# Optimization experiments

Measured on AMD Instinct MI355X. Metric: run time of the kernel, lower is better.

The kernel has to match this reference:

```python
import jax, jax.numpy as jnp
import numpy as np

NUM_NODES = 100000
NODE_FEAT_DIM = 512
EDGE_FEAT_DIM = 512
MEM_DIM = NODE_FEAT_DIM + EDGE_FEAT_DIM  # 1024
BATCH = 65536


def setup_inputs() -> dict:
    key = jax.random.key(0)
    k_ids, k_mem, k_emb, kq, ks, kk = jax.random.split(key, 6)
    scale = 1.0 / np.sqrt(MEM_DIM)
    inp = {
        "node_ids": jax.random.randint(k_ids, (BATCH,), 0, NUM_NODES, dtype=jnp.int64)
        if jax.config.jax_enable_x64 else
        jax.random.randint(k_ids, (BATCH,), 0, NUM_NODES, dtype=jnp.int32),
        # memory bank: (N, 1, D); randomized (instead of the zero init) so math is non-trivial
        "node_memories": jax.random.normal(k_mem, (NUM_NODES, 1, MEM_DIM), dtype=jnp.float32) * 0.02,
        "node_embedding": jax.random.normal(k_emb, (NUM_NODES, MEM_DIM), dtype=jnp.float32) * 0.02,
        "Wq": jax.random.normal(jax.random.fold_in(kq, 0), (MEM_DIM, NODE_FEAT_DIM), dtype=jnp.float32) * scale,
        "bq": jnp.zeros((NODE_FEAT_DIM,), dtype=jnp.float32),
        "Ws": jax.random.normal(jax.random.fold_in(ks, 0), (MEM_DIM, NODE_FEAT_DIM), dtype=jnp.float32) * scale,
        "bs": jnp.zeros((NODE_FEAT_DIM,), dtype=jnp.float32),
        "Wk": jax.random.normal(jax.random.fold_in(kk, 0), (MEM_DIM, NODE_FEAT_DIM), dtype=jnp.float32) * scale,
        "bk": jnp.zeros((NODE_FEAT_DIM,), dtype=jnp.float32),
    }
    return inp


def reference(node_ids, node_memories, node_embedding, Wq, bq, Ws, bs, Wk, bk):
    ids = node_ids.astype(jnp.int32)
    # torch.sum(node_memories[ids], dim=2): reduces feature dim -> (B, 1)
    mem_sum = jnp.sum(node_memories[ids], axis=2)          # (B, 1)
    x = mem_sum + node_embedding[ids]                      # broadcast -> (B, D)
    q = jax.nn.sigmoid(x @ Wq + bq)                        # (B, node_feat_dim)
    s = jax.nn.sigmoid(x @ Ws + bs)
    k = jax.nn.sigmoid(x @ Wk + bk)
    return (q, s, k)
```

## Files before the change

kernel.cpp:

```cpp
#include <hip/hip_runtime.h>
#include <hip/hip_bf16.h>
#include <stdint.h>

#define BATCH_N 65536
#define KDIM 1024
#define NTOT 1536

typedef __bf16 bf16x8 __attribute__((ext_vector_type(8)));
typedef float f32x4 __attribute__((ext_vector_type(4)));

__device__ __forceinline__ unsigned short f2bf(float f) {
    unsigned u = __builtin_bit_cast(unsigned, f);
    u += 0x7FFFu + ((u >> 16) & 1u);
    return (unsigned short)(u >> 16);
}

__global__ __launch_bounds__(256) void prep_kernel(
    const int* __restrict__ ids,
    const float* __restrict__ mem,
    const float* __restrict__ emb,
    unsigned short* __restrict__ x)
{
    const int b    = blockIdx.x * 4 + (threadIdx.x >> 6);
    const int lane = threadIdx.x & 63;
    const int id   = ids[b];
    const float4* m4 = (const float4*)(mem + (size_t)id * KDIM) + lane;
    const float4* e4 = (const float4*)(emb + (size_t)id * KDIM) + lane;
    float4 v0 = m4[0];
    float4 v1 = m4[64];
    float4 v2 = m4[128];
    float4 v3 = m4[192];
    float s = (v0.x + v0.y + v0.z + v0.w) + (v1.x + v1.y + v1.z + v1.w)
            + (v2.x + v2.y + v2.z + v2.w) + (v3.x + v3.y + v3.z + v3.w);
    #pragma unroll
    for (int off = 1; off < 64; off <<= 1) s += __shfl_xor(s, off, 64);
    unsigned short* xb = x + (size_t)b * KDIM;
    #pragma unroll
    for (int q = 0; q < 4; ++q) {
        float4 e = e4[q * 64];
        ushort4 o;
        o.x = f2bf(s + e.x);
        o.y = f2bf(s + e.y);
        o.z = f2bf(s + e.z);
        o.w = f2bf(s + e.w);
        const int k   = q * 256 + lane * 4;
        const int ksw = k ^ ((b & 7) << 3);
        *(ushort4*)(xb + ksw) = o;
    }
}

__global__ __launch_bounds__(256) void wconv_kernel(
    const float* __restrict__ Wq, const float* __restrict__ Ws,
    const float* __restrict__ Wk, unsigned short* __restrict__ wt)
{
    const int gt = blockIdx.x * 256 + threadIdx.x;
    const int n  = gt % NTOT;
    const int kb = (gt / NTOT) * 4;
    const float* W = (n < 512) ? Wq : ((n < 1024) ? Ws : Wk);
    const int nn = n & 511;
    ushort4 o;
    o.x = f2bf(W[(size_t)(kb + 0) * 512 + nn]);
    o.y = f2bf(W[(size_t)(kb + 1) * 512 + nn]);
    o.z = f2bf(W[(size_t)(kb + 2) * 512 + nn]);
    o.w = f2bf(W[(size_t)(kb + 3) * 512 + nn]);
    const int ksw = kb ^ ((n & 7) << 3);
    *(ushort4*)(wt + (size_t)n * KDIM + ksw) = o;
}

#define BM 256
#define BN 256
#define BK 64
#define MT (BATCH_N / BM)
#define NT (NTOT / BN)
#define NWG (MT * NT)

#define BAR() asm volatile("s_barrier" ::: "memory")
#define VM0() asm volatile("s_waitcnt vmcnt(0)" ::: "memory")
#define AS1 __attribute__((address_space(1)))
#define AS3 __attribute__((address_space(3)))

__global__ __launch_bounds__(512, 2) void gemm_kernel(
    const unsigned short* __restrict__ X,
    const unsigned short* __restrict__ Wt,
    const float* __restrict__ bq, const float* __restrict__ bs,
    const float* __restrict__ bk, float* __restrict__ out)
{
    __shared__ __align__(16) unsigned short sA[32768];
    __shared__ __align__(16) unsigned short sB[32768];

    const int tid  = threadIdx.x;
    const int xcd  = blockIdx.x & 7;
    const int idx  = blockIdx.x >> 3;
    const int wgid = xcd * (NWG / 8) + idx;
    const int nt   = wgid % NT;
    const int mt   = wgid / NT;
    const int m0   = mt * BM;
    const int n0   = nt * BN;
    const int wid  = tid >> 6;
    const int lane = tid & 63;
    const int wm   = wid >> 2;
    const int wn   = wid & 3;
    const int r16  = lane & 15;
    const int kb0  = (lane >> 4) << 4;
    const int ksw  = (r16 & 7) << 4;

    f32x4 acc[8][4];
    #pragma unroll
    for (int i = 0; i < 8; i++)
        #pragma unroll
        for (int j = 0; j < 4; j++)
            acc[i][j] = f32x4{0.f, 0.f, 0.f, 0.f};

    bf16x8 af0[4][2], af1[4][2], bfr0[2][2], bfr1[2][2];

    const unsigned short* gA = X  + (size_t)(m0 + (tid >> 3)) * KDIM + (tid & 7) * 8;
    const unsigned short* gB = Wt + (size_t)(n0 + (tid >> 3)) * KDIM + (tid & 7) * 8;
    const int ldst = (tid & 448) * 8;

#define STG_A(slot, h, kt) do {                                                 \
    _Pragma("unroll")                                                            \
    for (int c = 0; c < 2; ++c)                                                  \
        __builtin_amdgcn_global_load_lds(                                        \
            (const AS1 void*)(gA + (size_t)((h) * 128 + c * 64) * KDIM + (kt) * BK), \
            (AS3 void*)(&sA[((slot) * 2 + (h)) * 8192 + c * 4096 + ldst]),       \
            16, 0, 0);                                                           \
} while (0)
#define STG_B(slot, h, kt) do {                                                 \
    _Pragma("unroll")                                                            \
    for (int c = 0; c < 2; ++c)                                                  \
        __builtin_amdgcn_global_load_lds(                                        \
            (const AS1 void*)(gB + (size_t)((h) * 128 + c * 64) * KDIM + (kt) * BK), \
            (AS3 void*)(&sB[((slot) * 2 + (h)) * 8192 + c * 4096 + ldst]),       \
            16, 0, 0);                                                           \
} while (0)

#define LDA(SET, slot, qa) do {                                                 \
    const char* p = (const char*)&sA[((slot) * 2 + (qa)) * 8192];                \
    _Pragma("unroll")                                                            \
    for (int i = 0; i < 4; ++i)                                                  \
        _Pragma("unroll")                                                        \
        for (int kk = 0; kk < 2; ++kk)                                           \
            SET[i][kk] = *(const bf16x8*)(p + (wm * 64 + i * 16 + r16) * 128     \
                                            + ((kk * 64 + kb0) ^ ksw));          \
} while (0)
#define LDB(SET, slot, qb) do {                                                 \
    const char* p = (const char*)&sB[((slot) * 2 + (qb)) * 8192];                \
    _Pragma("unroll")                                                            \
    for (int j = 0; j < 2; ++j)                                                  \
        _Pragma("unroll")                                                        \
        for (int kk = 0; kk < 2; ++kk)                                           \
            SET[j][kk] = *(const bf16x8*)(p + (wn * 32 + j * 16 + r16) * 128     \
                                            + ((kk * 64 + kb0) ^ ksw));          \
} while (0)

#define MM(QA, QB, ASET, BSET) do {                                             \
    __builtin_amdgcn_s_setprio(1);                                               \
    _Pragma("unroll")                                                            \
    for (int i = 0; i < 4; ++i)                                                  \
        _Pragma("unroll")                                                        \
        for (int j = 0; j < 2; ++j)                                              \
            _Pragma("unroll")                                                    \
            for (int kk = 0; kk < 2; ++kk)                                       \
                acc[(QA) * 4 + i][(QB) * 2 + j] =                                \
                    __builtin_amdgcn_mfma_f32_16x16x32_bf16(                     \
                        ASET[i][kk], BSET[j][kk],                                \
                        acc[(QA) * 4 + i][(QB) * 2 + j], 0, 0, 0);               \
    __builtin_amdgcn_s_setprio(0);                                               \
} while (0)

#define TILE(S, NS, KTN, DOSTAGE) do {                                          \
    if (DOSTAGE) {                                                               \
        STG_A(NS, 0, KTN); STG_A(NS, 1, KTN);                                    \
        STG_B(NS, 0, KTN); STG_B(NS, 1, KTN);                                    \
    }                                                                            \
    LDA(af0, S, 0); LDB(bfr0, S, 0);                                             \
    LDA(af1, S, 1); LDB(bfr1, S, 1);                                             \
    MM(0, 0, af0, bfr0); MM(0, 1, af0, bfr1);                                    \
    MM(1, 1, af1, bfr1); MM(1, 0, af1, bfr0);                                    \
    VM0(); BAR();                                                                \
} while (0)

    STG_A(0, 0, 0); STG_A(0, 1, 0); STG_B(0, 0, 0); STG_B(0, 1, 0);
    VM0();
    BAR();

    #pragma unroll 1
    for (int t = 0; t < 7; ++t) {
        TILE(0, 1, 2 * t + 1, 1);
        TILE(1, 0, 2 * t + 2, 1);
    }
    TILE(0, 1, 15, 1);
    TILE(1, 0, 0, 0);

    const int grp = nt >> 1;
    const float* bias = (grp == 0) ? bq : ((grp == 1) ? bs : bk);
    float* obase = out + (size_t)grp * ((size_t)BATCH_N * 512);
    const int cb = (nt & 1) * 256;
    #pragma unroll
    for (int qb = 0; qb < 2; ++qb)
        #pragma unroll
        for (int j = 0; j < 2; ++j) {
            const int col = cb + qb * 128 + wn * 32 + j * 16 + r16;
            const float bv = bias[col];
            #pragma unroll
            for (int qa = 0; qa < 2; ++qa)
                #pragma unroll
                for (int i = 0; i < 4; ++i) {
                    const int rbase = m0 + qa * 128 + wm * 64 + i * 16 + ((lane >> 4) << 2);
                    #pragma unroll
                    for (int r = 0; r < 4; ++r) {
                        float v = acc[qa * 4 + i][qb * 2 + j][r] + bv;
                        v = 1.0f / (1.0f + __expf(-v));
                        __builtin_nontemporal_store(v, &obase[(size_t)(rbase + r) * 512 + col]);
                    }
                }
        }
#undef STG_A
#undef STG_B
#undef LDA
#undef LDB
#undef MM
#undef TILE
}

extern "C" void kernel_launch(void* const* d_in, const int* in_sizes, int n_in,
                              void* d_out, int out_size, void* d_ws, size_t ws_size,
                              hipStream_t stream) {
    const int*   ids = (const int*)d_in[0];
    const float* mem = (const float*)d_in[1];
    const float* emb = (const float*)d_in[2];
    const float* Wq  = (const float*)d_in[3];
    const float* bq  = (const float*)d_in[4];
    const float* Ws  = (const float*)d_in[5];
    const float* bs  = (const float*)d_in[6];
    const float* Wk  = (const float*)d_in[7];
    const float* bk  = (const float*)d_in[8];
    float* out = (float*)d_out;

    unsigned short* x  = (unsigned short*)d_ws;
    unsigned short* wt = x + (size_t)BATCH_N * KDIM;

    hipLaunchKernelGGL(wconv_kernel, dim3(NTOT), dim3(256), 0, stream, Wq, Ws, Wk, wt);
    hipLaunchKernelGGL(prep_kernel, dim3(BATCH_N / 4), dim3(256), 0, stream, ids, mem, emb, x);
    hipLaunchKernelGGL(gemm_kernel, dim3(NWG), dim3(512), 0, stream,
                       x, wt, bq, bs, bk, out);
}
```

Measured before the change: 432.6 us.

## Use 4-wave 256-thread GEMM blocks with 128x128 per-wave tiles

```diff
diff --git a/kernel.cpp b/kernel.cpp
--- a/kernel.cpp
+++ b/kernel.cpp
@@ -79,14 +79,14 @@
 #define AS1 __attribute__((address_space(1)))
 #define AS3 __attribute__((address_space(3)))
 
-__global__ __launch_bounds__(512, 2) void gemm_kernel(
+__global__ __launch_bounds__(256, 1) void gemm_kernel(
     const unsigned short* __restrict__ X,
     const unsigned short* __restrict__ Wt,
     const float* __restrict__ bq, const float* __restrict__ bs,
     const float* __restrict__ bk, float* __restrict__ out)
 {
-    __shared__ __align__(16) unsigned short sA[32768];
-    __shared__ __align__(16) unsigned short sB[32768];
+    __shared__ __align__(16) unsigned short sA[2 * 16384];
+    __shared__ __align__(16) unsigned short sB[2 * 16384];
 
     const int tid  = threadIdx.x;
     const int xcd  = blockIdx.x & 7;
@@ -98,128 +98,116 @@
     const int n0   = nt * BN;
     const int wid  = tid >> 6;
     const int lane = tid & 63;
-    const int wm   = wid >> 2;
-    const int wn   = wid & 3;
+    const int wm   = wid >> 1;
+    const int wn   = wid & 1;
     const int r16  = lane & 15;
     const int kb0  = (lane >> 4) << 4;
     const int ksw  = (r16 & 7) << 4;
 
-    f32x4 acc[8][4];
+    f32x4 acc[8][8];
     #pragma unroll
     for (int i = 0; i < 8; i++)
         #pragma unroll
-        for (int j = 0; j < 4; j++)
+        for (int j = 0; j < 8; j++)
             acc[i][j] = f32x4{0.f, 0.f, 0.f, 0.f};
 
-    bf16x8 af0[4][2], af1[4][2], bfr0[2][2], bfr1[2][2];
+    bf16x8 af[8][2], bfr[8][2];
 
     const unsigned short* gA = X  + (size_t)(m0 + (tid >> 3)) * KDIM + (tid & 7) * 8;
     const unsigned short* gB = Wt + (size_t)(n0 + (tid >> 3)) * KDIM + (tid & 7) * 8;
-    const int ldst = (tid & 448) * 8;
-
-#define STG_A(slot, h, kt) do {                                                 \
-    _Pragma("unroll")                                                            \
-    for (int c = 0; c < 2; ++c)                                                  \
+    const int ldst = (tid & 192) * 8;
+
+#define STG_A(slot, kt) do {                                                    \
+    _Pragma("unroll")                                                            \
+    for (int c = 0; c < 8; ++c)                                                  \
         __builtin_amdgcn_global_load_lds(                                        \
-            (const AS1 void*)(gA + (size_t)((h) * 128 + c * 64) * KDIM + (kt) * BK), \
-            (AS3 void*)(&sA[((slot) * 2 + (h)) * 8192 + c * 4096 + ldst]),       \
-            16, 0, 0);                                                           \
-} while (0)
-#define STG_B(slot, h, kt) do {                                                 \
-    _Pragma("unroll")                                                            \
-    for (int c = 0; c < 2; ++c)                                                  \
+            (const AS1 void*)(gA + (size_t)(c) * 32 * KDIM + (kt) * BK),         \
+            (AS3 void*)(&sA[(slot) * 16384 + (c) * 2048 + ldst]), 16, 0, 0);     \
+} while (0)
+#define STG_B(slot, kt) do {                                                    \
+    _Pragma("unroll")                                                            \
+    for (int c = 0; c < 8; ++c)                                                  \
         __builtin_amdgcn_global_load_lds(                                        \
-            (const AS1 void*)(gB + (size_t)((h) * 128 + c * 64) * KDIM + (kt) * BK), \
-            (AS3 void*)(&sB[((slot) * 2 + (h)) * 8192 + c * 4096 + ldst]),       \
-            16, 0, 0);                                                           \
-} while (0)
-
-#define LDA(SET, slot, qa) do {                                                 \
-    const char* p = (const char*)&sA[((slot) * 2 + (qa)) * 8192];                \
-    _Pragma("unroll")                                                            \
-    for (int i = 0; i < 4; ++i)                                                  \
+            (const AS1 void*)(gB + (size_t)(c) * 32 * KDIM + (kt) * BK),         \
+            (AS3 void*)(&sB[(slot) * 16384 + (c) * 2048 + ldst]), 16, 0, 0);     \
+} while (0)
+
+#define LDA1(slot, mf) do {                                                     \
+    const char* p = (const char*)&sA[(slot) * 16384];                            \
+    _Pragma("unroll")                                                            \
+    for (int kk = 0; kk < 2; ++kk)                                               \
+        af[mf][kk] = *(const bf16x8*)(p + (wm * 128 + (mf) * 16 + r16) * 128     \
+                                        + ((kk * 64 + kb0) ^ ksw));              \
+} while (0)
+#define LDB_ALL(slot) do {                                                      \
+    const char* p = (const char*)&sB[(slot) * 16384];                            \
+    _Pragma("unroll")                                                            \
+    for (int jf = 0; jf < 8; ++jf)                                               \
         _Pragma("unroll")                                                        \
         for (int kk = 0; kk < 2; ++kk)                                           \
-            SET[i][kk] = *(const bf16x8*)(p + (wm * 64 + i * 16 + r16) * 128     \
-                                            + ((kk * 64 + kb0) ^ ksw));          \
-} while (0)
-#define LDB(SET, slot, qb) do {                                                 \
-    const char* p = (const char*)&sB[((slot) * 2 + (qb)) * 8192];                \
-    _Pragma("unroll")                                                            \
-    for (int j = 0; j < 2; ++j)                                                  \
+            bfr[jf][kk] = *(const bf16x8*)(p + (wn * 128 + jf * 16 + r16) * 128  \
+                                             + ((kk * 64 + kb0) ^ ksw));         \
+} while (0)
+
+#define MMROW(mf) do {                                                          \
+    _Pragma("unroll")                                                            \
+    for (int jf = 0; jf < 8; ++jf)                                               \
         _Pragma("unroll")                                                        \
         for (int kk = 0; kk < 2; ++kk)                                           \
-            SET[j][kk] = *(const bf16x8*)(p + (wn * 32 + j * 16 + r16) * 128     \
-                                            + ((kk * 64 + kb0) ^ ksw));          \
-} while (0)
-
-#define MM(QA, QB, ASET, BSET) do {                                             \
-    __builtin_amdgcn_s_setprio(1);                                               \
-    _Pragma("unroll")                                                            \
-    for (int i = 0; i < 4; ++i)                                                  \
-        _Pragma("unroll")                                                        \
-        for (int j = 0; j < 2; ++j)                                              \
-            _Pragma("unroll")                                                    \
-            for (int kk = 0; kk < 2; ++kk)                                       \
-                acc[(QA) * 4 + i][(QB) * 2 + j] =                                \
-                    __builtin_amdgcn_mfma_f32_16x16x32_bf16(                     \
-                        ASET[i][kk], BSET[j][kk],                                \
-                        acc[(QA) * 4 + i][(QB) * 2 + j], 0, 0, 0);               \
-    __builtin_amdgcn_s_setprio(0);                                               \
-} while (0)
-
-#define TILE(S, NS, KTN, DOSTAGE) do {                                          \
-    if (DOSTAGE) {                                                               \
-        STG_A(NS, 0, KTN); STG_A(NS, 1, KTN);                                    \
-        STG_B(NS, 0, KTN); STG_B(NS, 1, KTN);                                    \
-    }                                                                            \
-    LDA(af0, S, 0); LDB(bfr0, S, 0);                                             \
-    LDA(af1, S, 1); LDB(bfr1, S, 1);                                             \
-    MM(0, 0, af0, bfr0); MM(0, 1, af0, bfr1);                                    \
-    MM(1, 1, af1, bfr1); MM(1, 0, af1, bfr0);                                    \
+            acc[mf][jf] = __builtin_amdgcn_mfma_f32_16x16x32_bf16(               \
+                af[mf][kk], bfr[jf][kk], acc[mf][jf], 0, 0, 0);                  \
+} while (0)
+
+#define TILE(S, KTN, DOSTAGE) do {                                              \
+    if (DOSTAGE) { STG_A((S) ^ 1, KTN); STG_B((S) ^ 1, KTN); }                   \
+    LDB_ALL(S);                                                                  \
+    LDA1(S, 0); LDA1(S, 1);                                                      \
+    LDA1(S, 2); MMROW(0);                                                        \
+    LDA1(S, 3); MMROW(1);                                                        \
+    LDA1(S, 4); MMROW(2);                                                        \
+    LDA1(S, 5); MMROW(3);                                                        \
+    LDA1(S, 6); MMROW(4);                                                        \
+    LDA1(S, 7); MMROW(5);                                                        \
+    MMROW(6); MMROW(7);                                                          \
     VM0(); BAR();                                                                \
 } while (0)
 
-    STG_A(0, 0, 0); STG_A(0, 1, 0); STG_B(0, 0, 0); STG_B(0, 1, 0);
+    STG_A(0, 0); STG_B(0, 0);
     VM0();
     BAR();
 
     #pragma unroll 1
     for (int t = 0; t < 7; ++t) {
-        TILE(0, 1, 2 * t + 1, 1);
-        TILE(1, 0, 2 * t + 2, 1);
+        TILE(0, 2 * t + 1, 1);
+        TILE(1, 2 * t + 2, 1);
     }
-    TILE(0, 1, 15, 1);
-    TILE(1, 0, 0, 0);
+    TILE(0, 15, 1);
+    TILE(1, 0, 0);
 
     const int grp = nt >> 1;
     const float* bias = (grp == 0) ? bq : ((grp == 1) ? bs : bk);
     float* obase = out + (size_t)grp * ((size_t)BATCH_N * 512);
     const int cb = (nt & 1) * 256;
     #pragma unroll
-    for (int qb = 0; qb < 2; ++qb)
+    for (int jf = 0; jf < 8; ++jf) {
+        const int col = cb + wn * 128 + jf * 16 + r16;
+        const float bv = bias[col];
         #pragma unroll
-        for (int j = 0; j < 2; ++j) {
-            const int col = cb + qb * 128 + wn * 32 + j * 16 + r16;
-            const float bv = bias[col];
+        for (int mf = 0; mf < 8; ++mf) {
+            const int rbase = m0 + wm * 128 + mf * 16 + ((lane >> 4) << 2);
             #pragma unroll
-            for (int qa = 0; qa < 2; ++qa)
-                #pragma unroll
-                for (int i = 0; i < 4; ++i) {
-                    const int rbase = m0 + qa * 128 + wm * 64 + i * 16 + ((lane >> 4) << 2);
-                    #pragma unroll
-                    for (int r = 0; r < 4; ++r) {
-                        float v = acc[qa * 4 + i][qb * 2 + j][r] + bv;
-                        v = 1.0f / (1.0f + __expf(-v));
-                        __builtin_nontemporal_store(v, &obase[(size_t)(rbase + r) * 512 + col]);
-                    }
-                }
+            for (int r = 0; r < 4; ++r) {
+                float v = acc[mf][jf][r] + bv;
+                v = 1.0f / (1.0f + __expf(-v));
+                __builtin_nontemporal_store(v, &obase[(size_t)(rbase + r) * 512 + col]);
+            }
         }
+    }
 #undef STG_A
 #undef STG_B
-#undef LDA
-#undef LDB
-#undef MM
+#undef LDA1
+#undef LDB_ALL
+#undef MMROW
 #undef TILE
 }
 
@@ -242,6 +230,6 @@
 
     hipLaunchKernelGGL(wconv_kernel, dim3(NTOT), dim3(256), 0, stream, Wq, Ws, Wk, wt);
     hipLaunchKernelGGL(prep_kernel, dim3(BATCH_N / 4), dim3(256), 0, stream, ids, mem, emb, x);
-    hipLaunchKernelGGL(gemm_kernel, dim3(NWG), dim3(512), 0, stream,
+    hipLaunchKernelGGL(gemm_kernel, dim3(NWG), dim3(256), 0, stream,
                        x, wt, bq, bs, bk, out);
 }
```

New measurement: 496.2 us. 1.15x slower.
